# Performance work log

Hardware: AMD Instinct MI355X
Metric: run time of the kernel (lower is better)

Reference implementation:

```python
import jax, jax.numpy as jnp
import numpy as np

B, N, D_IN, H, D_OUT = 64, 512, 1024, 1024, 1024
EPS = 1e-5          # torch BatchNorm1d default eps
NEG_SLOPE = 0.01    # torch leaky_relu default


def setup_inputs() -> dict:
    key = jax.random.key(0)
    ks = jax.random.split(key, 12)
    s_in = 1.0 / np.sqrt(D_IN)
    s_h = 1.0 / np.sqrt(H)
    return {
        "x": jax.random.normal(ks[0], (B, N, D_IN), dtype=jnp.float32),
        # weights stored as [in, out] so y = x @ W + b
        "W1": jax.random.uniform(ks[1], (D_IN, H), jnp.float32, -s_in, s_in),
        "b1": jax.random.uniform(ks[2], (H,), jnp.float32, -s_in, s_in),
        "gamma": jnp.ones((N,), jnp.float32),
        "beta": jnp.zeros((N,), jnp.float32),
        "W2": jax.random.uniform(ks[3], (D_IN, H), jnp.float32, -s_in, s_in),
        "b2": jax.random.uniform(ks[4], (H,), jnp.float32, -s_in, s_in),
        "W3": jax.random.uniform(ks[5], (H, D_OUT), jnp.float32, -s_h, s_h),
        "b3": jax.random.uniform(ks[6], (D_OUT,), jnp.float32, -s_h, s_h),
        "W4": jax.random.uniform(ks[7], (D_IN, D_OUT), jnp.float32, -s_in, s_in),
        "b4": jax.random.uniform(ks[8], (D_OUT,), jnp.float32, -s_in, s_in),
    }


def reference(x, W1, b1, gamma, beta, W2, b2, W3, b3, W4, b4):
    h = W1.shape[1]
    # theta_x = leaky_relu(bn(l1(x)))
    t = x @ W1 + b1                                   # [B, N, H]
    # BatchNorm1d(num_input): channel dim is N; train-mode batch stats over (B, H)
    mean = jnp.mean(t, axis=(0, 2), keepdims=True)
    var = jnp.var(t, axis=(0, 2), keepdims=True)      # biased variance (torch norm path)
    t = gamma[None, :, None] * (t - mean) * jax.lax.rsqrt(var + EPS) + beta[None, :, None]
    t = jnp.where(t >= 0, t, NEG_SLOPE * t)
    # sigma = theta @ M @ theta^T with M = (I - 1/h)/h  ==  mean-center rows then scale by 1/h
    tM = (t - jnp.mean(t, axis=-1, keepdims=True)) / h  # [B, N, H]
    sigma = jnp.einsum("bnh,bmh->bnm", tM, t)           # [B, N, N]
    att = sigma / jnp.sqrt(jnp.float32(h))              # normal_factor = sqrt(hidden)
    # GLOBAL softmax over the full flattened N*N matrix per batch element
    bsz, n = x.shape[0], x.shape[1]
    att = jax.nn.softmax(att.reshape(bsz, -1), axis=1).reshape(bsz, n, n)
    g = x @ W2 + b2                                     # [B, N, H]
    p = jnp.einsum("bnm,bmh->bnh", att, g) @ W3 + b3    # [B, N, D_OUT]
    phi = x @ W4 + b4                                   # [B, N, D_OUT]
    return phi + p
```

## Files before the change

### kernel.cpp

```cpp
#include <hip/hip_runtime.h>
#include <hip/hip_bf16.h>

typedef _Float16 f16x8 __attribute__((ext_vector_type(8)));
typedef _Float16 f16x4 __attribute__((ext_vector_type(4)));
typedef float    f32x4 __attribute__((ext_vector_type(4)));

#define EPS_ 1e-5f

__device__ __forceinline__ void gload_lds16(const _Float16* g, _Float16* l) {
    __builtin_amdgcn_global_load_lds(
        (const __attribute__((address_space(1))) void*)g,
        (__attribute__((address_space(3))) void*)l, 16, 0, 0);
}


__global__ void k_cvt_f16(const float* __restrict__ in, _Float16* __restrict__ out, int n4) {
    int i = blockIdx.x * blockDim.x + threadIdx.x;
    int stride = gridDim.x * blockDim.x;
    const float4* in4 = (const float4*)in;
    for (; i < n4; i += stride) {
        float4 v = in4[i];
        f16x4 o;
        o[0] = (_Float16)v.x; o[1] = (_Float16)v.y;
        o[2] = (_Float16)v.z; o[3] = (_Float16)v.w;
        *(f16x4*)(out + (size_t)i * 4) = o;
    }
}

__global__ void k_transpose_w(const float* __restrict__ in, _Float16* __restrict__ out) {
    __shared__ float tile[32][33];
    int bx = blockIdx.x * 32;
    int by = blockIdx.y * 32;
    int tx = threadIdx.x, ty = threadIdx.y;
    #pragma unroll
    for (int r = 0; r < 32; r += 8)
        tile[ty + r][tx] = in[(size_t)(by + ty + r) * 1024 + bx + tx];
    __syncthreads();
    #pragma unroll
    for (int r = 0; r < 32; r += 8)
        out[(size_t)(bx + ty + r) * 1024 + by + tx] = (_Float16)tile[tx][ty + r];
}

__global__ void k_b23(const float* __restrict__ b2, const float* __restrict__ W3,
                      float* __restrict__ b23) {
    const int oo = threadIdx.x & 63, hc = threadIdx.x >> 6;
    const int o = blockIdx.x * 64 + oo;
    float s = 0.f;
    for (int h = hc * 256; h < hc * 256 + 256; ++h) s += b2[h] * W3[(size_t)h * 1024 + o];
    __shared__ float red[4][64];
    red[hc][oo] = s;
    __syncthreads();
    if (threadIdx.x < 64) {
        int o2 = blockIdx.x * 64 + threadIdx.x;
        b23[o2] = red[0][threadIdx.x] + red[1][threadIdx.x] + red[2][threadIdx.x] + red[3][threadIdx.x];
    }
}


__global__ void k_bnstats(const _Float16* __restrict__ t, const float* __restrict__ gamma,
                          const float* __restrict__ beta, float* __restrict__ scale,
                          float* __restrict__ shift) {
    const int n = blockIdx.x, tid = threadIdx.x;
    float s = 0.f, s2 = 0.f;
    const _Float16* base = t + (size_t)n * 1024 + tid * 4;
    for (int b = 0; b < 64; ++b) {
        f16x4 v = *(const f16x4*)(base + (size_t)b * 512 * 1024);
        float x0 = (float)v[0], x1 = (float)v[1], x2 = (float)v[2], x3 = (float)v[3];
        s  += x0 + x1 + x2 + x3;
        s2 += x0 * x0 + x1 * x1 + x2 * x2 + x3 * x3;
    }
    #pragma unroll
    for (int o = 32; o > 0; o >>= 1) { s += __shfl_down(s, o); s2 += __shfl_down(s2, o); }
    __shared__ float rs_[4], rs2_[4];
    int lane = tid & 63, w = tid >> 6;
    if (lane == 0) { rs_[w] = s; rs2_[w] = s2; }
    __syncthreads();
    if (tid == 0) {
        float S  = rs_[0] + rs_[1] + rs_[2] + rs_[3];
        float S2 = rs2_[0] + rs2_[1] + rs2_[2] + rs2_[3];
        float mean = S * (1.f / 65536.f);
        float var  = S2 * (1.f / 65536.f) - mean * mean;
        float r = rsqrtf(var + EPS_);
        float sc = gamma[n] * r;
        scale[n] = sc;
        shift[n] = beta[n] - mean * sc;
    }
}

__global__ void k_bnorm(const _Float16* __restrict__ t, const float* __restrict__ scale,
                        const float* __restrict__ shift, _Float16* __restrict__ theta,
                        float* __restrict__ mu) {
    const int row = blockIdx.x, tid = threadIdx.x;
    const int n = row & 511;
    const float sc = scale[n], sh = shift[n];
    f16x4 v = *(const f16x4*)(t + (size_t)row * 1024 + tid * 4);
    float a0 = fmaf((float)v[0], sc, sh); a0 = a0 >= 0.f ? a0 : 0.01f * a0;
    float a1 = fmaf((float)v[1], sc, sh); a1 = a1 >= 0.f ? a1 : 0.01f * a1;
    float a2 = fmaf((float)v[2], sc, sh); a2 = a2 >= 0.f ? a2 : 0.01f * a2;
    float a3 = fmaf((float)v[3], sc, sh); a3 = a3 >= 0.f ? a3 : 0.01f * a3;
    float s = a0 + a1 + a2 + a3;
    #pragma unroll
    for (int o = 32; o > 0; o >>= 1) s += __shfl_down(s, o);
    __shared__ float red[4];
    int lane = tid & 63, w = tid >> 6;
    if (lane == 0) red[w] = s;
    __syncthreads();
    const float mean = (red[0] + red[1] + red[2] + red[3]) * (1.f / 1024.f);
    f16x4 th;
    th[0] = (_Float16)a0; th[1] = (_Float16)a1; th[2] = (_Float16)a2; th[3] = (_Float16)a3;
    *(f16x4*)(theta + (size_t)row * 1024 + tid * 4) = th;
    if (tid == 0) mu[row] = mean;
}

__global__ void k_ssum(const float* __restrict__ part, float* __restrict__ rsum,
                       float* __restrict__ ssum) {
    const int b = blockIdx.x, j = threadIdx.x;
    const int idx = b * 512 + j;
    float s = part[idx] + part[32768 + idx] + part[65536 + idx] + part[98304 + idx];
    rsum[idx] = s;
    #pragma unroll
    for (int o = 32; o > 0; o >>= 1) s += __shfl_down(s, o);
    __shared__ float red[8];
    if ((j & 63) == 0) red[j >> 6] = s;
    __syncthreads();
    if (j == 0) {
        float tt = 0.f;
        #pragma unroll
        for (int k = 0; k < 8; k++) tt += red[k];
        ssum[b] = tt;
    }
}


template <int MODE>
__global__ __launch_bounds__(256) void k_gemm(
    const _Float16* __restrict__ A0, const _Float16* __restrict__ B0,
    const float* __restrict__ auxA, float* __restrict__ auxW,
    void* __restrict__ outp) {

    constexpr int BK = 32;
    __shared__ _Float16 Al[4096];
    __shared__ _Float16 Bl[4096];

    const int tid = threadIdx.x, lane = tid & 63, w = tid >> 6;
    const int wm = w >> 1, wn = w & 1;
    const int bm = blockIdx.x, bn = blockIdx.y, bz = blockIdx.z;

    const int srow = tid >> 2;
    const int skofs = ((tid & 3) ^ ((tid >> 3) & 3)) * 8;
    _Float16* lA0 = &Al[(w * 64) * 8];
    _Float16* lA1 = &Al[(256 + w * 64) * 8];
    _Float16* lB0 = &Bl[(w * 64) * 8];
    _Float16* lB1 = &Bl[(256 + w * 64) * 8];

    const int lr = lane & 15, kg = lane >> 4;
    const int kswz = kg ^ ((lr >> 1) & 3);

    f32x4 acc[4][4] = {};

    const size_t aO = ((size_t)bz * 512 + bm * 128) * 1024;
    const size_t bO = ((size_t)bz * 512 + bn * 128) * 1024;
    for (int k0 = 0; k0 < 1024; k0 += BK) {
        gload_lds16(A0 + aO + (size_t)srow * 1024 + k0 + skofs, lA0);
        gload_lds16(A0 + aO + (size_t)(srow + 64) * 1024 + k0 + skofs, lA1);
        gload_lds16(B0 + bO + (size_t)srow * 1024 + k0 + skofs, lB0);
        gload_lds16(B0 + bO + (size_t)(srow + 64) * 1024 + k0 + skofs, lB1);
        __syncthreads();
        f16x8 af[4], bf[4];
        #pragma unroll
        for (int m = 0; m < 4; m++)
            af[m] = *(const f16x8*)&Al[((wm * 64 + m * 16 + lr) * 4 + kswz) * 8];
        #pragma unroll
        for (int n = 0; n < 4; n++)
            bf[n] = *(const f16x8*)&Bl[((wn * 64 + n * 16 + lr) * 4 + kswz) * 8];
        #pragma unroll
        for (int m = 0; m < 4; m++)
            #pragma unroll
            for (int n = 0; n < 4; n++)
                acc[m][n] = __builtin_amdgcn_mfma_f32_16x16x32_f16(af[m], bf[n], acc[m][n], 0, 0, 0);
        __syncthreads();
    }

    if constexpr (MODE == 1) {
        __shared__ float rbuf[2][128];
        _Float16* o = (_Float16*)outp + (size_t)bz * 262144;
        #pragma unroll
        for (int m = 0; m < 4; m++) {
            const int r0 = wm * 64 + m * 16 + kg * 4;
            float rs[4] = {0.f, 0.f, 0.f, 0.f};
            #pragma unroll
            for (int n = 0; n < 4; n++) {
                const int gc = bn * 128 + wn * 64 + n * 16 + lr;
                const float mj = auxA[bz * 512 + gc];
                #pragma unroll
                for (int i = 0; i < 4; i++) {
                    const float mi = auxA[bz * 512 + bm * 128 + r0 + i];
                    const float e = __expf(acc[m][n][i] * (1.f / 32768.f) - mi * mj * (1.f / 32.f));
                    o[(size_t)(bm * 128 + r0 + i) * 512 + gc] = (_Float16)e;
                    rs[i] += e;
                }
            }
            #pragma unroll
            for (int i = 0; i < 4; i++) {
                float v = rs[i];
                v += __shfl_xor(v, 1); v += __shfl_xor(v, 2);
                v += __shfl_xor(v, 4); v += __shfl_xor(v, 8);
                if (lr == 0) rbuf[wn][r0 + i] = v;
            }
        }
        __syncthreads();
        if (tid < 128)
            auxW[(size_t)bn * 32768 + bz * 512 + bm * 128 + tid] = rbuf[0][tid] + rbuf[1][tid];
    } else {
        _Float16* o = (_Float16*)outp;
        #pragma unroll
        for (int m = 0; m < 4; m++) {
            #pragma unroll
            for (int n = 0; n < 4; n++) {
                const int r0 = wm * 64 + m * 16 + kg * 4;
                const int gc = bn * 128 + wn * 64 + n * 16 + lr;
                #pragma unroll
                for (int i = 0; i < 4; i++)
                    o[(size_t)(bm * 128 + r0 + i) * 1024 + gc] = (_Float16)acc[m][n][i];
            }
        }
    }
}


template <int MODE>
__global__ __launch_bounds__(512) void k_gemm8(
    const _Float16* __restrict__ A0, const _Float16* __restrict__ B0,
    const _Float16* __restrict__ A1, const _Float16* __restrict__ B1,
    const float* __restrict__ biasf, const float* __restrict__ biasg,
    const float* __restrict__ auxA, const float* __restrict__ auxB,
    const float* __restrict__ sumptr, void* __restrict__ outp) {

    __shared__ _Float16 LA[32768];
    __shared__ _Float16 LB[32768];

    const int tid = threadIdx.x, lane = tid & 63, wid = tid >> 6;
    const int wm = wid >> 2, wn = wid & 3;
    const int lr = lane & 15, kq = lane >> 4;

    const int swz = (blockIdx.x & 7) * 64 + (blockIdx.x >> 3);
    int bm, bn, bz = 0;
    if constexpr (MODE == 3) { bz = swz >> 3; bm = (swz >> 2) & 1; bn = swz & 3; }
    else { bm = swz >> 2; bn = swz & 3; }

    constexpr int NITER = (MODE == 3) ? 12 : 8;
    float oscale = 1.f;
    if constexpr (MODE == 3) oscale = 1.f / sumptr[bz];

    const int i0 = tid >> 3;
    const int kgs = (tid & 7) ^ (i0 & 7);

    auto STAGE = [&](int g, int isA, int h) {
        const _Float16* P; int ld; size_t off; int kk;
        if constexpr (MODE == 3) {
            if (g < 8) {
                kk = g * 64;
                if (isA) { P = A0; ld = 512;  off = (size_t)bz * 262144 + (size_t)bm * 256 * 512; }
                else     { P = B0; ld = 512;  off = (size_t)bz * 524288 + (size_t)bn * 256 * 512; }
            } else {
                kk = (g - 8) * 64;
                if (isA) { P = A1; ld = 1024; off = ((size_t)bz * 512 + bm * 256) * 1024; }
                else     { P = B1; ld = 1024; off = (size_t)bn * 256 * 1024; }
            }
        } else {
            kk = g * 64;
            if (isA) { P = A0; ld = 1024; off = (size_t)bm * 256 * 1024; }
            else     { P = B0; ld = 1024; off = (size_t)bn * 256 * 1024; }
        }
        const int l0 = isA ? (h * 64 + i0)
                           : ((i0 >> 5) * 64 + h * 32 + (i0 & 31));
        const int l1 = isA ? (128 + h * 64 + i0)
                           : (((i0 >> 5) + 2) * 64 + h * 32 + (i0 & 31));
        _Float16* dst = (isA ? LA : LB) + ((g & 1) * 2 + h) * 8192 + wid * 512;
        gload_lds16(P + off + (size_t)l0 * ld + kk + kgs * 8, dst);
        gload_lds16(P + off + (size_t)l1 * ld + kk + kgs * 8, dst + 4096);
    };

    f32x4 acc[8][4] = {};

    STAGE(0, 1, 0); STAGE(0, 0, 0); STAGE(0, 1, 1); STAGE(0, 0, 1);
    STAGE(1, 1, 0); STAGE(1, 0, 0);
    asm volatile("s_waitcnt vmcnt(4)" ::: "memory");
    __builtin_amdgcn_s_barrier();

    for (int i = 0; i < NITER; ++i) {
        if constexpr (MODE == 3) {
            if (i == 4) {
                #pragma unroll
                for (int m = 0; m < 8; m++)
                    #pragma unroll
                    for (int n = 0; n < 4; n++)
                        #pragma unroll
                        for (int v = 0; v < 4; v++) acc[m][n][v] *= oscale;
            }
        }
        const bool more = (i + 1 < NITER);
        #pragma unroll
        for (int ph = 0; ph < 8; ++ph) {
            const int kt = ph >> 2, qm = (ph >> 1) & 1, qn = ph & 1;
            const _Float16* As = LA + (kt * 2 + qm) * 8192;
            const _Float16* Bs = LB + (kt * 2 + qn) * 8192;
            f16x8 af[4][2], bf[2][2];
            #pragma unroll
            for (int j = 0; j < 4; j++)
                #pragma unroll
                for (int s = 0; s < 2; s++)
                    af[j][s] = *(const f16x8*)&As[(wm * 64 + j * 16 + lr) * 64
                                                  + ((((s << 2) | kq) ^ (lr & 7)) << 3)];
            #pragma unroll
            for (int jj = 0; jj < 2; jj++)
                #pragma unroll
                for (int s = 0; s < 2; s++)
                    bf[jj][s] = *(const f16x8*)&Bs[(wn * 32 + jj * 16 + lr) * 64
                                                   + ((((s << 2) | kq) ^ (lr & 7)) << 3)];
            {
                const int gadd = 1 + ((ph + 2) >> 2);
                const int sh = ((ph >> 1) & 1) ^ 1;
                const int sA = (ph & 1) ^ 1;
                if (ph < 2 || more) STAGE(2 * i + gadd, sA, sh);
            }
            __builtin_amdgcn_s_barrier();
            asm volatile("s_waitcnt lgkmcnt(0)" ::: "memory");
            __builtin_amdgcn_sched_barrier(0);
            __builtin_amdgcn_s_setprio(1);
            #pragma unroll
            for (int j = 0; j < 4; j++)
                #pragma unroll
                for (int jj = 0; jj < 2; jj++)
                    #pragma unroll
                    for (int s = 0; s < 2; s++)
                        acc[qm * 4 + j][qn * 2 + jj] = __builtin_amdgcn_mfma_f32_16x16x32_f16(
                            af[j][s], bf[jj][s], acc[qm * 4 + j][qn * 2 + jj], 0, 0, 0);
            __builtin_amdgcn_s_setprio(0);
            if (ph == 3) {
                if (more) asm volatile("s_waitcnt vmcnt(4)" ::: "memory");
                else      asm volatile("s_waitcnt vmcnt(0)" ::: "memory");
            }
            if (ph == 7 && more) asm volatile("s_waitcnt vmcnt(4)" ::: "memory");
            __builtin_amdgcn_s_barrier();
        }
    }

    #pragma unroll
    for (int m = 0; m < 8; m++) {
        #pragma unroll
        for (int n = 0; n < 4; n++) {
            const int gc = bn * 256 + wn * 64 + n * 16 + lr;
            const int gr0 = bm * 256 + wm * 128 + m * 16 + kq * 4;
            if constexpr (MODE == 0) {
                _Float16* o = (_Float16*)outp;
                const float bias = biasf[gc];
                #pragma unroll
                for (int i = 0; i < 4; i++)
                    o[(size_t)(gr0 + i) * 1024 + gc] = (_Float16)(acc[m][n][i] + bias);
            } else if constexpr (MODE == 2) {
                _Float16* o = (_Float16*)outp;
                const int bb = gr0 >> 9, mm = gr0 & 511;
                f16x4 pk;
                #pragma unroll
                for (int i = 0; i < 4; i++) pk[i] = (_Float16)acc[m][n][i];
                *(f16x4*)(o + ((size_t)bb * 1024 + gc) * 512 + mm) = pk;
            } else {
                float* o = (float*)outp;
                const float tail = biasf[gc] + biasg[gc];
                const float b23v = auxB[gc];
                #pragma unroll
                for (int i = 0; i < 4; i++) {
                    const int row = gr0 + i;
                    o[((size_t)bz * 512 + row) * 1024 + gc] =
                        acc[m][n][i] + auxA[bz * 512 + row] * oscale * b23v + tail;
                }
            }
        }
    }
}


extern "C" void kernel_launch(void* const* d_in, const int* in_sizes, int n_in,
                              void* d_out, int out_size, void* d_ws, size_t ws_size,
                              hipStream_t stream) {
    (void)in_sizes; (void)n_in; (void)out_size; (void)ws_size;
    const float* x     = (const float*)d_in[0];
    const float* W1    = (const float*)d_in[1];
    const float* b1    = (const float*)d_in[2];
    const float* gamma = (const float*)d_in[3];
    const float* beta  = (const float*)d_in[4];
    const float* W2    = (const float*)d_in[5];
    const float* b2    = (const float*)d_in[6];
    const float* W3    = (const float*)d_in[7];
    const float* b3    = (const float*)d_in[8];
    const float* W4    = (const float*)d_in[9];
    const float* b4    = (const float*)d_in[10];

    char* wsb = (char*)d_ws;
    const size_t MB = 1024 * 1024;
    _Float16* xb    = (_Float16*)(wsb);
    _Float16* W1t   = (_Float16*)(wsb + 64 * MB);
    _Float16* W3t   = (_Float16*)(wsb + 66 * MB);
    _Float16* W4t   = (_Float16*)(wsb + 68 * MB);
    _Float16* W2h   = (_Float16*)(wsb + 70 * MB);
    _Float16* W23t  = (_Float16*)(wsb + 72 * MB);
    float*    b23   = (float*)(wsb + 74 * MB);
    float*    scl   = (float*)(wsb + 74 * MB + 8192);
    float*    shf   = (float*)(wsb + 74 * MB + 16384);
    float*    ssum  = (float*)(wsb + 74 * MB + 24576);
    float*    mu    = (float*)(wsb + 75 * MB);
    float*    rsum  = (float*)(wsb + 76 * MB);
    float*    rpart = (float*)(wsb + 77 * MB);
    _Float16* t     = (_Float16*)(wsb + 80 * MB);
    _Float16* theta = (_Float16*)(wsb + 144 * MB);
    _Float16* att   = (_Float16*)(wsb + 208 * MB);
    _Float16* gwt   = (_Float16*)(wsb + 240 * MB);

    k_cvt_f16<<<8192, 256, 0, stream>>>(x, xb, 64 * 512 * 1024 / 4);
    k_cvt_f16<<<1024, 256, 0, stream>>>(W2, W2h, 1024 * 1024 / 4);
    dim3 tb(32, 8), tg(32, 32);
    k_transpose_w<<<tg, tb, 0, stream>>>(W1, W1t);
    k_transpose_w<<<tg, tb, 0, stream>>>(W3, W3t);
    k_transpose_w<<<tg, tb, 0, stream>>>(W4, W4t);
    k_gemm<5><<<dim3(8, 8, 1), 256, 0, stream>>>(W3t, W2h, nullptr, nullptr, W23t);
    k_b23<<<16, 256, 0, stream>>>(b2, W3, b23);
    k_gemm8<0><<<512, 512, 0, stream>>>(xb, W1t, nullptr, nullptr,
        b1, nullptr, nullptr, nullptr, nullptr, t);
    k_bnstats<<<512, 256, 0, stream>>>(t, gamma, beta, scl, shf);
    k_bnorm<<<32768, 256, 0, stream>>>(t, scl, shf, theta, mu);
    k_gemm<1><<<dim3(4, 4, 64), 256, 0, stream>>>(theta, theta, mu, rpart, att);
    k_ssum<<<64, 512, 0, stream>>>(rpart, rsum, ssum);
    k_gemm8<2><<<512, 512, 0, stream>>>(xb, W23t, nullptr, nullptr,
        nullptr, nullptr, nullptr, nullptr, nullptr, gwt);
    k_gemm8<3><<<512, 512, 0, stream>>>(att, gwt, xb, W4t,
        b3, b4, rsum, b23, ssum, d_out);
}
```

Baseline: 503.3 us.

## Restructure GEMM main loop to load B fragments once per k-tile with deeper prefetch

The 8-phase inner loop, where each phase reloaded both A and B fragments for a 4x2 quadrant, is replaced by a k-tile loop that loads all B fragments once and then walks four A sub-blocks of 2 rows x 4 columns. This cuts LDS reads per k-tile. The global-to-LDS staging schedule is also reordered and given one more stage in the prologue, with matching vmcnt thresholds, so more loads stay in flight. The cost is more live B-fragment registers, and the hand-tuned waitcnt/stage ordering is fragile to get right.

```diff
diff --git a/kernel.cpp b/kernel.cpp
--- a/kernel.cpp
+++ b/kernel.cpp
@@ -283,9 +283,9 @@
 
     f32x4 acc[8][4] = {};
 
-    STAGE(0, 1, 0); STAGE(0, 0, 0); STAGE(0, 1, 1); STAGE(0, 0, 1);
-    STAGE(1, 1, 0); STAGE(1, 0, 0);
-    asm volatile("s_waitcnt vmcnt(4)" ::: "memory");
+    STAGE(0, 1, 0); STAGE(0, 0, 0); STAGE(0, 0, 1); STAGE(0, 1, 1);
+    STAGE(1, 0, 0); STAGE(1, 0, 1); STAGE(1, 1, 0);
+    asm volatile("s_waitcnt vmcnt(6)" ::: "memory");
     __builtin_amdgcn_s_barrier();
 
     for (int i = 0; i < NITER; ++i) {
@@ -301,48 +301,59 @@
         }
         const bool more = (i + 1 < NITER);
         #pragma unroll
-        for (int ph = 0; ph < 8; ++ph) {
-            const int kt = ph >> 2, qm = (ph >> 1) & 1, qn = ph & 1;
-            const _Float16* As = LA + (kt * 2 + qm) * 8192;
-            const _Float16* Bs = LB + (kt * 2 + qn) * 8192;
-            f16x8 af[4][2], bf[2][2];
+        for (int kt = 0; kt < 2; ++kt) {
+            f16x8 bf[4][2];
             #pragma unroll
-            for (int j = 0; j < 4; j++)
-                #pragma unroll
-                for (int s = 0; s < 2; s++)
-                    af[j][s] = *(const f16x8*)&As[(wm * 64 + j * 16 + lr) * 64
-                                                  + ((((s << 2) | kq) ^ (lr & 7)) << 3)];
-            #pragma unroll
-            for (int jj = 0; jj < 2; jj++)
-                #pragma unroll
-                for (int s = 0; s < 2; s++)
-                    bf[jj][s] = *(const f16x8*)&Bs[(wn * 32 + jj * 16 + lr) * 64
-                                                   + ((((s << 2) | kq) ^ (lr & 7)) << 3)];
-            {
-                const int gadd = 1 + ((ph + 2) >> 2);
-                const int sh = ((ph >> 1) & 1) ^ 1;
-                const int sA = (ph & 1) ^ 1;
-                if (ph < 2 || more) STAGE(2 * i + gadd, sA, sh);
-            }
-            __builtin_amdgcn_s_barrier();
-            asm volatile("s_waitcnt lgkmcnt(0)" ::: "memory");
-            __builtin_amdgcn_sched_barrier(0);
-            __builtin_amdgcn_s_setprio(1);
-            #pragma unroll
-            for (int j = 0; j < 4; j++)
-                #pragma unroll
-                for (int jj = 0; jj < 2; jj++)
+            for (int sub = 0; sub < 4; ++sub) {
+                const int ph = kt * 4 + sub;
+                if (sub == 0) {
+                    #pragma unroll
+                    for (int n = 0; n < 4; n++) {
+                        const _Float16* Bs = LB + (kt * 2 + (n >> 1)) * 8192;
+                        #pragma unroll
+                        for (int s = 0; s < 2; s++)
+                            bf[n][s] = *(const f16x8*)&Bs[(wn * 32 + (n & 1) * 16 + lr) * 64
+                                                           + ((((s << 2) | kq) ^ (lr & 7)) << 3)];
+                    }
+                }
+                const _Float16* As = LA + (kt * 2 + (sub >> 1)) * 8192;
+                f16x8 af[2][2];
+                #pragma unroll
+                for (int j = 0; j < 2; j++) {
+                    const int m = sub * 2 + j;
                     #pragma unroll
                     for (int s = 0; s < 2; s++)
-                        acc[qm * 4 + j][qn * 2 + jj] = __builtin_amdgcn_mfma_f32_16x16x32_f16(
-                            af[j][s], bf[jj][s], acc[qm * 4 + j][qn * 2 + jj], 0, 0, 0);
-            __builtin_amdgcn_s_setprio(0);
-            if (ph == 3) {
-                if (more) asm volatile("s_waitcnt vmcnt(4)" ::: "memory");
-                else      asm volatile("s_waitcnt vmcnt(0)" ::: "memory");
-            }
-            if (ph == 7 && more) asm volatile("s_waitcnt vmcnt(4)" ::: "memory");
-            __builtin_amdgcn_s_barrier();
+                        af[j][s] = *(const f16x8*)&As[(wm * 64 + (m & 3) * 16 + lr) * 64
+                                                       + ((((s << 2) | kq) ^ (lr & 7)) << 3)];
+                }
+                {
+                    constexpr int gof[8] = {1, 2, 2, 2, 2, 3, 3, 3};
+                    constexpr int isa[8] = {1, 0, 0, 1, 1, 0, 0, 1};
+                    constexpr int hh [8] = {1, 0, 1, 0, 1, 0, 1, 0};
+                    if (ph == 0 || more) STAGE(2 * i + gof[ph], isa[ph], hh[ph]);
+                }
+                __builtin_amdgcn_s_barrier();
+                asm volatile("s_waitcnt lgkmcnt(0)" ::: "memory");
+                __builtin_amdgcn_sched_barrier(0);
+                __builtin_amdgcn_s_setprio(1);
+                #pragma unroll
+                for (int j = 0; j < 2; j++)
+                    #pragma unroll
+                    for (int n = 0; n < 4; n++)
+                        #pragma unroll
+                        for (int s = 0; s < 2; s++)
+                            acc[sub * 2 + j][n] = __builtin_amdgcn_mfma_f32_16x16x32_f16(
+                                af[j][s], bf[n][s], acc[sub * 2 + j][n], 0, 0, 0);
+                __builtin_amdgcn_s_setprio(0);
+                if (ph == 1) { if (more) asm volatile("s_waitcnt vmcnt(10)" ::: "memory");
+                               else      asm volatile("s_waitcnt vmcnt(8)"  ::: "memory"); }
+                if (ph == 3) { if (more) asm volatile("s_waitcnt vmcnt(8)"  ::: "memory");
+                               else      asm volatile("s_waitcnt vmcnt(2)"  ::: "memory"); }
+                if (ph == 5) { if (more) asm volatile("s_waitcnt vmcnt(10)" ::: "memory");
+                               else      asm volatile("s_waitcnt vmcnt(0)"  ::: "memory"); }
+                if (ph == 7) { if (more) asm volatile("s_waitcnt vmcnt(8)"  ::: "memory"); }
+                __builtin_amdgcn_s_barrier();
+            }
         }
     }
 
```

After: 463.2 us. 8.0% less time.
